# Performance work log

Measured on AMD Instinct MI355X. Metric: run time of the kernel, lower is better.

Reference implementation:

```python
import jax, jax.numpy as jnp
import numpy as np

B, S, D_IN, D_OUT = 4, 2048, 1024, 1024


def setup_inputs() -> dict:
    key = jax.random.key(0)
    k1, k2, k3, k4 = jax.random.split(key, 4)
    scale = 1.0 / np.sqrt(D_IN)
    return {
        "x": jax.random.normal(k1, (B, S, D_IN), dtype=jnp.float32),
        # torch nn.Linear weights have shape [d_out, d_in]
        "Wq": jax.random.normal(k2, (D_OUT, D_IN), dtype=jnp.float32) * scale,
        "Wk": jax.random.normal(k3, (D_OUT, D_IN), dtype=jnp.float32) * scale,
        "Wv": jax.random.normal(k4, (D_OUT, D_IN), dtype=jnp.float32) * scale,
    }


def reference(x, Wq, Wk, Wv):
    # Linear projections (torch Linear: y = x @ W.T), no bias
    q = jnp.einsum('bsd,od->bso', x, Wq)
    k = jnp.einsum('bsd,od->bso', x, Wk)
    v = jnp.einsum('bsd,od->bso', x, Wv)
    s = q.shape[1]
    scores = jnp.einsum('bqd,bkd->bqk', q, k)  # [B, S, S]
    causal = jnp.tril(jnp.ones((s, s), dtype=bool))  # True = keep
    scores = jnp.where(causal[None], scores, -jnp.inf)
    scale = jnp.asarray(k.shape[-1], scores.dtype) ** 0.5
    weights = jax.nn.softmax(scores / scale, axis=-1)
    return jnp.einsum('bqk,bkd->bqd', weights, v)
```

## Files before the change

kernel.cpp:

```cpp
#include <hip/hip_runtime.h>

#define BATCH 4
#define SEQ   2048
#define DIM   1024
#define MTOT  (BATCH * SEQ)
#define BK    32

typedef __bf16 bf16x8 __attribute__((ext_vector_type(8)));
typedef __bf16 bf16x4 __attribute__((ext_vector_type(4)));
typedef float  f32x4  __attribute__((ext_vector_type(4)));

#define VMCNT(N) asm volatile("s_waitcnt vmcnt(" #N ")" ::: "memory")

__device__ __forceinline__ void gl_lds16(const __bf16* g, __bf16* l) {
    __builtin_amdgcn_global_load_lds(
        (const __attribute__((address_space(1))) void*)g,
        (__attribute__((address_space(3))) void*)l,
        16, 0, 0);
}

__global__ __launch_bounds__(256) void cvt_all_kernel(
    const float* __restrict__ x,  const float* __restrict__ w0,
    const float* __restrict__ w1, const float* __restrict__ w2,
    __bf16* __restrict__ xd, __bf16* __restrict__ d0,
    __bf16* __restrict__ d1, __bf16* __restrict__ d2,
    float* __restrict__ sums)
{
    const int bid = blockIdx.x;
    if (bid >= 5632) {
        const int i = ((bid - 5632) * 256 + threadIdx.x) * 4;
        *(float4*)(sums + i) = (float4){0.f, 0.f, 0.f, 0.f};
        return;
    }
    const float* s;
    __bf16* d;
    int base;
    if (bid < 4096)      { s = x;  d = xd; base = bid; }
    else if (bid < 4608) { s = w0; d = d0; base = bid - 4096; }
    else if (bid < 5120) { s = w1; d = d1; base = bid - 4608; }
    else                 { s = w2; d = d2; base = bid - 5120; }
    const int i = (base * 256 + threadIdx.x) * 8;
    const float4 a = *(const float4*)(s + i);
    const float4 b = *(const float4*)(s + i + 4);
    bf16x8 o;
    o[0] = (__bf16)a.x; o[1] = (__bf16)a.y; o[2] = (__bf16)a.z; o[3] = (__bf16)a.w;
    o[4] = (__bf16)b.x; o[5] = (__bf16)b.y; o[6] = (__bf16)b.z; o[7] = (__bf16)b.w;
    *(bf16x8*)(d + i) = o;
}

__device__ __forceinline__ void gemm_core(
    const __bf16* __restrict__ A, size_t lda,
    const __bf16* __restrict__ Bm, size_t ldb,
    int m0, int n0, int kTiles,
    __bf16* lA, __bf16* lB,
    f32x4 (&acc)[4][4])
{
    const int tid  = threadIdx.x;
    const int lane = tid & 63;
    const int wave = tid >> 6;
    const int wm = (wave >> 1) << 6;
    const int wn = (wave & 1) << 6;

#pragma unroll
    for (int i = 0; i < 4; ++i)
#pragma unroll
        for (int j = 0; j < 4; ++j)
            acc[i][j] = (f32x4){0.f, 0.f, 0.f, 0.f};

    for (int kt = 0; kt < kTiles; ++kt) {
        const int k0 = kt << 5;
        __syncthreads();
#pragma unroll
        for (int it = 0; it < 2; ++it) {
            const int f   = tid + (it << 8);
            const int row = f >> 2;
            const int col = (f & 3) << 3;
            gl_lds16(A  + (size_t)(m0 + row) * lda + (size_t)(k0 + col), lA + f * 8);
            gl_lds16(Bm + (size_t)(n0 + row) * ldb + (size_t)(k0 + col), lB + f * 8);
        }
        __syncthreads();

        bf16x8 af[4], bfr[4];
#pragma unroll
        for (int i = 0; i < 4; ++i) {
            af[i]  = *(const bf16x8*)(lA + (size_t)(wm + i * 16 + (lane & 15)) * BK + ((lane >> 4) << 3));
            bfr[i] = *(const bf16x8*)(lB + (size_t)(wn + i * 16 + (lane & 15)) * BK + ((lane >> 4) << 3));
        }
#pragma unroll
        for (int i = 0; i < 4; ++i)
#pragma unroll
            for (int j = 0; j < 4; ++j)
                acc[i][j] = __builtin_amdgcn_mfma_f32_16x16x32_bf16(af[i], bfr[j], acc[i][j], 0, 0, 0);
    }
}

__device__ __forceinline__ void store_tile_bf16(
    f32x4 (&acc)[4][4], __bf16* scratch, bool transpose, float scale,
    __bf16* dst, size_t ldo, size_t r0, size_t c0,
    bool expMask = false, bool diag = false, float* sums = nullptr)
{
    const int tid  = threadIdx.x;
    const int lane = tid & 63;
    const int wave = tid >> 6;
    const int wm = (wave >> 1) << 6, wn = (wave & 1) << 6;
    const int quad = lane >> 4;
    const int ln15 = lane & 15;

#pragma unroll
    for (int p = 0; p < 4; ++p) {
        __syncthreads();
        if (!transpose) {
            if (wm == ((p >> 1) << 6)) {
#pragma unroll
                for (int ih = 0; ih < 2; ++ih) {
                    const int i = ((p & 1) << 1) + ih;
                    const int lr = ih * 16 + quad * 4;
#pragma unroll
                    for (int r = 0; r < 4; ++r) {
                        const int lm = wm + ((p & 1) << 5) + lr + r;
                        float ps = 0.f;
#pragma unroll
                        for (int j = 0; j < 4; ++j) {
                            const int ln = wn + j * 16 + ln15;
                            float v = acc[i][j][r] * scale;
                            if (expMask) {
                                v = (!diag || ln <= lm) ? __expf(v) : 0.f;
                            }
                            const __bf16 vb = (__bf16)v;
                            scratch[(lr + r) * 136 + ln] = vb;
                            ps += (float)vb;
                        }
                        if (sums) {
#pragma unroll
                            for (int off = 1; off < 16; off <<= 1)
                                ps += __shfl_xor(ps, off);
                            if (ln15 == 0)
                                atomicAdd(&sums[r0 + (p << 5) + lr + r], ps);
                        }
                    }
                }
            }
        } else {
            if (wn == ((p >> 1) << 6)) {
#pragma unroll
                for (int jh = 0; jh < 2; ++jh) {
                    const int j = ((p & 1) << 1) + jh;
                    const int lr = jh * 16 + ln15;
#pragma unroll
                    for (int i = 0; i < 4; ++i)
#pragma unroll
                        for (int r = 0; r < 4; ++r)
                            scratch[lr * 136 + wm + i * 16 + quad * 4 + r] =
                                (__bf16)(acc[i][j][r] * scale);
                }
            }
        }
        __syncthreads();
#pragma unroll
        for (int it = 0; it < 2; ++it) {
            const int g   = tid + (it << 8);
            const int row = g >> 4;
            const int col = (g & 15) << 3;
            *(bf16x8*)(dst + (r0 + p * 32 + row) * ldo + c0 + col) =
                *(const bf16x8*)(scratch + row * 136 + col);
        }
    }
}

__global__ __launch_bounds__(512, 2) void qkv_kernel(
    const __bf16* __restrict__ x,
    const __bf16* __restrict__ Wq,
    const __bf16* __restrict__ Wk,
    const __bf16* __restrict__ Wv,
    __bf16* __restrict__ Q, __bf16* __restrict__ Kb, __bf16* __restrict__ Vt)
{
    __shared__ __bf16 smem[49152];

    const int L  = blockIdx.x;
    const int g  = (L & 7) * 32 + (L >> 3);
    const int m0 = (g >> 3) << 8;
    const int B3 = g & 7;

    const int tid  = threadIdx.x;
    const int lane = tid & 63;
    const int ln15 = lane & 15;
    const int quad = lane >> 4;
    const int wave = tid >> 6;
    const int wm   = wave >> 1;
    const int wn   = wave & 1;

    const int r0  = tid >> 3;
    const int cst = ((((tid & 7) + 8) - (r0 & 7)) & 7) << 3;
    const int cq  = (((quad << 3) + ((ln15 & 7) << 3)) & 63);

    int aoff[4];
#pragma unroll
    for (int i = 0; i < 4; ++i)
        aoff[i] = ((wm >> 1) ? 8192 : 0) + (((wm & 1) << 6) + i * 16 + ln15) * 64 + cq;
    int boff[4];
#pragma unroll
    for (int j = 0; j < 4; ++j)
        boff[j] = 16384 + (wn ? 4096 : 0) + (j * 16 + ln15) * 64 + cq;

    const __bf16* Ab = x + (size_t)m0 * DIM;
    constexpr int nt = DIM / 64;

    for (int uu = 0; uu < 3; ++uu) {
        const int u  = B3 * 3 + uu;
        const int z  = u >> 3;
        const int n0 = (u & 7) << 7;
        const __bf16* W  = (z == 0) ? Wq : (z == 1) ? Wk : Wv;
        const __bf16* Bb = W + (size_t)n0 * DIM;

        f32x4 acc[4][4];
#pragma unroll
        for (int i = 0; i < 4; ++i)
#pragma unroll
            for (int j = 0; j < 4; ++j) acc[i][j] = (f32x4){0.f, 0.f, 0.f, 0.f};

#define SA(h, t) do {                                                         \
    const __bf16* gs_ = Ab + (size_t)((h) * 128 + r0) * DIM + ((t) << 6) + cst; \
    __bf16* ls_ = smem + (((t) & 1) * 24576 + (h) * 8192) + tid * 8;          \
    gl_lds16(gs_, ls_);                                                       \
    gl_lds16(gs_ + (size_t)64 * DIM, ls_ + 4096); } while (0)
#define SB(h, t) do {                                                         \
    const __bf16* gs_ = Bb + (size_t)((h) * 64 + r0) * DIM + ((t) << 6) + cst; \
    __bf16* ls_ = smem + (((t) & 1) * 24576 + 16384 + (h) * 4096) + tid * 8;  \
    gl_lds16(gs_, ls_); } while (0)

        bf16x8 aFa[4][2], aFb[4][2], bFr[2][2];
#define LDA_LO(DST, t) do { const __bf16* p_ = smem + ((t) & 1) * 24576;      \
    DST[0][0] = *(const bf16x8*)(p_ + aoff[0]);                               \
    DST[0][1] = *(const bf16x8*)(p_ + (aoff[0] ^ 32));                        \
    DST[1][0] = *(const bf16x8*)(p_ + aoff[1]);                               \
    DST[1][1] = *(const bf16x8*)(p_ + (aoff[1] ^ 32)); } while (0)
#define LDA_HI(DST, t) do { const __bf16* p_ = smem + ((t) & 1) * 24576;      \
    DST[2][0] = *(const bf16x8*)(p_ + aoff[2]);                               \
    DST[2][1] = *(const bf16x8*)(p_ + (aoff[2] ^ 32));                        \
    DST[3][0] = *(const bf16x8*)(p_ + aoff[3]);                               \
    DST[3][1] = *(const bf16x8*)(p_ + (aoff[3] ^ 32)); } while (0)
#define LDB(s, j, t) do { const __bf16* p_ = smem + ((t) & 1) * 24576;        \
    bFr[s][0] = *(const bf16x8*)(p_ + boff[j]);                               \
    bFr[s][1] = *(const bf16x8*)(p_ + (boff[j] ^ 32)); } while (0)
#define MG(j, s, AC) do {                                                     \
    __builtin_amdgcn_s_setprio(1);                                            \
    _Pragma("unroll") for (int i_ = 0; i_ < 4; ++i_) {                        \
        acc[i_][j] = __builtin_amdgcn_mfma_f32_16x16x32_bf16(                 \
            AC[i_][0], bFr[s][0], acc[i_][j], 0, 0, 0);                       \
        acc[i_][j] = __builtin_amdgcn_mfma_f32_16x16x32_bf16(                 \
            AC[i_][1], bFr[s][1], acc[i_][j], 0, 0, 0); }                     \
    __builtin_amdgcn_s_setprio(0); } while (0)

#define TILE(AC, AN, T) do {                                                  \
                       \
    LDB(1, 1, T);                                                             \
    if ((T) + 1 < nt) SB(0, (T) + 1);                                         \
    __builtin_amdgcn_s_barrier();                                             \
    MG(0, 0, AC);                                                             \
    __builtin_amdgcn_s_barrier();                                             \
      \
    LDB(0, 2, T);                                                             \
    if ((T) + 1 < nt) SB(1, (T) + 1);                                         \
    if ((T) + 2 < nt) SA(0, (T) + 2);                                         \
    if ((T) + 1 < nt) { if ((T) + 2 < nt) VMCNT(4); else VMCNT(2); }          \
    __builtin_amdgcn_s_barrier();                                             \
    MG(1, 1, AC);                                                             \
    __builtin_amdgcn_s_barrier();                                             \
      \
    LDB(1, 3, T);                                                             \
    if ((T) + 1 < nt) LDA_LO(AN, (T) + 1);                                    \
    if ((T) + 2 < nt) SA(1, (T) + 2);                                         \
    if ((T) + 1 < nt) { if ((T) + 2 < nt) VMCNT(5); else VMCNT(1); }          \
    __builtin_amdgcn_s_barrier();                                             \
    MG(2, 0, AC);                                                             \
    __builtin_amdgcn_s_barrier();                                             \
           \
    if ((T) + 1 < nt) { LDA_HI(AN, (T) + 1); LDB(0, 0, (T) + 1); }            \
    if ((T) + 1 < nt) { if ((T) + 2 < nt) VMCNT(4); else VMCNT(0); }          \
    __builtin_amdgcn_s_barrier();                                             \
    MG(3, 1, AC);                                                             \
    __builtin_amdgcn_s_barrier(); } while (0)

        SA(0, 0); SA(1, 0); SB(0, 0); SB(1, 0);
        SA(0, 1); SA(1, 1);
        VMCNT(4);
        __builtin_amdgcn_s_barrier();
        LDA_LO(aFa, 0); LDA_HI(aFa, 0); LDB(0, 0, 0);

#pragma unroll 1
        for (int T = 0; T < nt; T += 2) {
            TILE(aFa, aFb, T);
            TILE(aFb, aFa, T + 1);
        }
#undef SA
#undef SB
#undef LDA_LO
#undef LDA_HI
#undef LDB
#undef MG
#undef TILE

        __syncthreads();
        __bf16* scratch = smem;

        if (z < 2) {
            __bf16* dst = (z == 0) ? Q : Kb;
#pragma unroll
            for (int h = 0; h < 2; ++h) {
                if ((wm >> 1) == h) {
#pragma unroll
                    for (int i = 0; i < 4; ++i) {
                        const int lr = ((wm & 1) << 6) + i * 16 + quad * 4;
#pragma unroll
                        for (int j = 0; j < 4; ++j) {
                            const int lc = (wn << 6) + j * 16 + ln15;
#pragma unroll
                            for (int r = 0; r < 4; ++r)
                                scratch[(lr + r) * 136 + lc] = (__bf16)acc[i][j][r];
                        }
                    }
                }
                __syncthreads();
#pragma unroll
                for (int it = 0; it < 4; ++it) {
                    const int f = tid + (it << 9);
                    const int row = f >> 4, col = (f & 15) << 3;
                    *(bf16x8*)(dst + (size_t)(m0 + h * 128 + row) * DIM + n0 + col) =
                        *(const bf16x8*)(scratch + row * 136 + col);
                }
                __syncthreads();
            }
        } else {
            const size_t b  = (size_t)(m0 >> 11);
            const int  ms0  = m0 & (SEQ - 1);
            __bf16* dst = Vt + b * (size_t)DIM * SEQ;
#pragma unroll
            for (int i = 0; i < 4; ++i) {
                const int sl = (wm << 6) + i * 16 + quad * 4;
#pragma unroll
                for (int j = 0; j < 4; ++j) {
                    const int dl = (wn << 6) + j * 16 + ln15;
                    bf16x4 v;
#pragma unroll
                    for (int r = 0; r < 4; ++r) v[r] = (__bf16)acc[i][j][r];
                    *(bf16x4*)(scratch + dl * 264 + sl) = v;
                }
            }
            __syncthreads();
#pragma unroll
            for (int it = 0; it < 8; ++it) {
                const int f = tid + (it << 9);
                const int row = f >> 5, blk = f & 31;
                *(bf16x8*)(dst + (size_t)(n0 + row) * SEQ + ms0 + blk * 8) =
                    *(const bf16x8*)(scratch + row * 264 + blk * 8);
            }
            __syncthreads();
        }
    }
}

__global__ __launch_bounds__(256) void scores_kernel(
    const __bf16* __restrict__ Q, const __bf16* __restrict__ Kb,
    __bf16* __restrict__ Sc, float* __restrict__ sums)
{
    const int L = blockIdx.x;
    const int g = (L & 7) * 68 + (L >> 3);
    const int b = g / 136;
    const int t = g - b * 136;
    int i = (int)((sqrtf(8.f * t + 1.f) - 1.f) * 0.5f);
    while ((i + 1) * (i + 2) / 2 <= t) ++i;
    while (i * (i + 1) / 2 > t) --i;
    const int j = t - i * (i + 1) / 2;

    __shared__ __bf16 smem[8192];
    __bf16* lA = smem;
    __bf16* lB = smem + 128 * BK;
    const __bf16* A  = Q  + (size_t)b * SEQ * DIM;
    const __bf16* Bm = Kb + (size_t)b * SEQ * DIM;

    f32x4 acc[4][4];
    gemm_core(A, DIM, Bm, DIM, i << 7, j << 7, DIM / BK, lA, lB, acc);

    store_tile_bf16(acc, smem, false, 0.03125f,
                    Sc + (size_t)b * SEQ * SEQ, SEQ,
                    (size_t)(i << 7), (size_t)(j << 7),
                    true, (i == j),
                    sums + (size_t)b * SEQ);
}

__global__ __launch_bounds__(256) void pv_kernel(
    const __bf16* __restrict__ P, const __bf16* __restrict__ Vt,
    const float* __restrict__ sums, float* __restrict__ out)
{
    const int L = blockIdx.x;
    const int c = L & 7;
    const int k = L >> 3;
    const int b = c >> 1;
    const int i = 15 - (c & 1) - ((k >> 3) << 1);
    const int x = k & 7;

    __shared__ __bf16 smem[8192];
    __bf16* lA = smem;
    __bf16* lB = smem + 128 * BK;
    const __bf16* A  = P  + (size_t)b * SEQ * SEQ;
    const __bf16* Bm = Vt + (size_t)b * DIM * SEQ;

    f32x4 acc[4][4];
    gemm_core(A, SEQ, Bm, SEQ, i << 7, x << 7, (i + 1) * (128 / BK), lA, lB, acc);

    const int lane = threadIdx.x & 63;
    const int wave = threadIdx.x >> 6;
    const int wm = (wave >> 1) << 6, wn = (wave & 1) << 6;
#pragma unroll
    for (int ii = 0; ii < 4; ++ii)
#pragma unroll
        for (int jj = 0; jj < 4; ++jj)
#pragma unroll
            for (int r = 0; r < 4; ++r) {
                const int m = (i << 7) + wm + ii * 16 + ((lane >> 4) << 2) + r;
                const int n = (x << 7) + wn + jj * 16 + (lane & 15);
                out[((size_t)b * SEQ + m) * DIM + n] =
                    acc[ii][jj][r] / sums[(b << 11) + m];
            }
}

extern "C" void kernel_launch(void* const* d_in, const int* in_sizes, int n_in,
                              void* d_out, int out_size, void* d_ws, size_t ws_size,
                              hipStream_t stream) {
    const float* x  = (const float*)d_in[0];
    const float* Wq = (const float*)d_in[1];
    const float* Wk = (const float*)d_in[2];
    const float* Wv = (const float*)d_in[3];
    float* out = (float*)d_out;

    char* ws = (char*)d_ws;
    __bf16* Q  = (__bf16*)(ws);
    __bf16* Kb = (__bf16*)(ws + (16ull << 20));
    __bf16* Vt = (__bf16*)(ws + (32ull << 20));
    __bf16* Sc = (__bf16*)(ws + (48ull << 20));
    __bf16* Wqb = (__bf16*)(ws + (80ull << 20));
    __bf16* Wkb = (__bf16*)(ws + (82ull << 20));
    __bf16* Wvb = (__bf16*)(ws + (84ull << 20));
    float*  sums = (float*)(ws + (86ull << 20));
    __bf16* xb  = (__bf16*)d_out;

    cvt_all_kernel<<<dim3(5640), 256, 0, stream>>>(x, Wq, Wk, Wv, xb, Wqb, Wkb, Wvb, sums);

    qkv_kernel    <<<dim3(256),  512, 0, stream>>>(xb, Wqb, Wkb, Wvb, Q, Kb, Vt);
    scores_kernel <<<dim3(544),  256, 0, stream>>>(Q, Kb, Sc, sums);
    pv_kernel     <<<dim3(512),  256, 0, stream>>>(Sc, Vt, sums, out);
}
```

Before: 230.9 us.

## Move PV GEMM onto shared 256x128 pipelined unit_gemm with zeroed diagonal padding

Extracts the QKV kernel's 256x128 tile GEMM mainloop into a reusable unit_gemm with a simpler double-buffered schedule. The PV kernel now uses it, with 512-thread blocks and 256-row tiles that cover the causal range in 64-wide K steps. The convert kernel gains extra blocks that zero the upper-diagonal 128x128 score blocks, which the larger row tiles now read but scores_kernel never writes. The QKV mainloop loses its register double-buffered A fragments and finer interleaving, which may reduce its overlap.

```diff
diff --git a/kernel.cpp b/kernel.cpp
--- a/kernel.cpp
+++ b/kernel.cpp
@@ -24,9 +24,23 @@
     const float* __restrict__ w1, const float* __restrict__ w2,
     __bf16* __restrict__ xd, __bf16* __restrict__ d0,
     __bf16* __restrict__ d1, __bf16* __restrict__ d2,
-    float* __restrict__ sums)
+    float* __restrict__ sums, __bf16* __restrict__ Sc)
 {
     const int bid = blockIdx.x;
+    if (bid >= 5640) {
+        const int t  = bid - 5640;
+        const int bb = t >> 3, i2 = t & 7;
+        __bf16* base = Sc + (size_t)bb * SEQ * SEQ
+                          + (size_t)(i2 * 256) * SEQ + (i2 * 256 + 128);
+        const bf16x8 z8 = {};
+#pragma unroll
+        for (int it = 0; it < 8; ++it) {
+            const int row = it * 16 + (threadIdx.x >> 4);
+            const int col = (threadIdx.x & 15) << 3;
+            *(bf16x8*)(base + (size_t)row * SEQ + col) = z8;
+        }
+        return;
+    }
     if (bid >= 5632) {
         const int i = ((bid - 5632) * 256 + threadIdx.x) * 4;
         *(float4*)(sums + i) = (float4){0.f, 0.f, 0.f, 0.f};
@@ -167,20 +181,11 @@
     }
 }
 
-__global__ __launch_bounds__(512, 2) void qkv_kernel(
-    const __bf16* __restrict__ x,
-    const __bf16* __restrict__ Wq,
-    const __bf16* __restrict__ Wk,
-    const __bf16* __restrict__ Wv,
-    __bf16* __restrict__ Q, __bf16* __restrict__ Kb, __bf16* __restrict__ Vt)
-{
-    __shared__ __bf16 smem[49152];
-
-    const int L  = blockIdx.x;
-    const int g  = (L & 7) * 32 + (L >> 3);
-    const int m0 = (g >> 3) << 8;
-    const int B3 = g & 7;
-
+__device__ __forceinline__ void unit_gemm(
+    const __bf16* __restrict__ Ab, size_t lda,
+    const __bf16* __restrict__ Bb, size_t ldb,
+    int nt, __bf16* smem, f32x4 (&acc)[4][4])
+{
     const int tid  = threadIdx.x;
     const int lane = tid & 63;
     const int ln15 = lane & 15;
@@ -188,117 +193,115 @@
     const int wave = tid >> 6;
     const int wm   = wave >> 1;
     const int wn   = wave & 1;
-
-    const int r0  = tid >> 3;
-    const int cst = ((((tid & 7) + 8) - (r0 & 7)) & 7) << 3;
-    const int cq  = (((quad << 3) + ((ln15 & 7) << 3)) & 63);
-
-    int aoff[4];
+    const int r0   = tid >> 3;
+    const int cst  = ((((tid & 7) + 8) - (r0 & 7)) & 7) << 3;
+    const int cq   = (((quad << 3) + ((ln15 & 7) << 3)) & 63);
+
+    int aoff[4], boff[4];
+#pragma unroll
+    for (int i = 0; i < 4; ++i) aoff[i] = ((wm << 6) + i * 16 + ln15) * 64 + cq;
+#pragma unroll
+    for (int j = 0; j < 4; ++j) boff[j] = 16384 + ((wn << 6) + j * 16 + ln15) * 64 + cq;
+
 #pragma unroll
     for (int i = 0; i < 4; ++i)
-        aoff[i] = ((wm >> 1) ? 8192 : 0) + (((wm & 1) << 6) + i * 16 + ln15) * 64 + cq;
-    int boff[4];
-#pragma unroll
-    for (int j = 0; j < 4; ++j)
-        boff[j] = 16384 + (wn ? 4096 : 0) + (j * 16 + ln15) * 64 + cq;
+#pragma unroll
+        for (int j = 0; j < 4; ++j) acc[i][j] = (f32x4){0.f, 0.f, 0.f, 0.f};
+
+    bf16x8 aF[4][2], bFr[2][2];
+
+#define SA(h, t) do {                                                         \
+    const __bf16* gs_ = Ab + (size_t)((h) * 128 + r0) * lda + ((t) << 6) + cst; \
+    __bf16* ls_ = smem + (((t) & 1) * 24576 + (h) * 8192) + tid * 8;          \
+    gl_lds16(gs_, ls_);                                                       \
+    gl_lds16(gs_ + (size_t)64 * lda, ls_ + 4096); } while (0)
+#define SB(h, t) do {                                                         \
+    const __bf16* gs_ = Bb + (size_t)((h) * 64 + r0) * ldb + ((t) << 6) + cst; \
+    __bf16* ls_ = smem + (((t) & 1) * 24576 + 16384 + (h) * 4096) + tid * 8;  \
+    gl_lds16(gs_, ls_); } while (0)
+#define LDA_ALL(t) do { const __bf16* p_ = smem + ((t) & 1) * 24576;          \
+    _Pragma("unroll") for (int i_ = 0; i_ < 4; ++i_) {                        \
+        aF[i_][0] = *(const bf16x8*)(p_ + aoff[i_]);                          \
+        aF[i_][1] = *(const bf16x8*)(p_ + (aoff[i_] ^ 32)); } } while (0)
+#define LDB2(s, j, t) do { const __bf16* p_ = smem + ((t) & 1) * 24576;       \
+    bFr[s][0] = *(const bf16x8*)(p_ + boff[j]);                               \
+    bFr[s][1] = *(const bf16x8*)(p_ + (boff[j] ^ 32)); } while (0)
+#define MG(j, s) do {                                                         \
+    _Pragma("unroll") for (int i_ = 0; i_ < 4; ++i_) {                        \
+        acc[i_][j] = __builtin_amdgcn_mfma_f32_16x16x32_bf16(                 \
+            aF[i_][0], bFr[s][0], acc[i_][j], 0, 0, 0);                       \
+        acc[i_][j] = __builtin_amdgcn_mfma_f32_16x16x32_bf16(                 \
+            aF[i_][1], bFr[s][1], acc[i_][j], 0, 0, 0); } } while (0)
+
+    SA(0, 0); SA(1, 0); SB(0, 0); SB(1, 0);
+    SA(0, 1); SA(1, 1);
+    VMCNT(4);
+    __builtin_amdgcn_s_barrier();
+
+    for (int T = 0; T < nt; ++T) {
+        LDA_ALL(T);
+        LDB2(0, 0, T); LDB2(1, 1, T);
+        if (T + 1 < nt) {
+            SB(0, T + 1); SB(1, T + 1);
+            VMCNT(2);
+        }
+        __builtin_amdgcn_s_barrier();
+        __builtin_amdgcn_s_setprio(1);
+        MG(0, 0); MG(1, 1);
+        __builtin_amdgcn_s_setprio(0);
+        __builtin_amdgcn_s_barrier();
+        LDB2(0, 2, T); LDB2(1, 3, T);
+        if (T + 2 < nt) {
+            SA(0, T + 2); SA(1, T + 2);
+            VMCNT(4);
+        } else if (T + 1 < nt) {
+            VMCNT(0);
+        }
+        __builtin_amdgcn_s_barrier();
+        __builtin_amdgcn_s_setprio(1);
+        MG(2, 0); MG(3, 1);
+        __builtin_amdgcn_s_setprio(0);
+        __builtin_amdgcn_s_barrier();
+    }
+#undef SA
+#undef SB
+#undef LDA_ALL
+#undef LDB2
+#undef MG
+}
+
+__global__ __launch_bounds__(512, 2) void qkv_kernel(
+    const __bf16* __restrict__ x,
+    const __bf16* __restrict__ Wq,
+    const __bf16* __restrict__ Wk,
+    const __bf16* __restrict__ Wv,
+    __bf16* __restrict__ Q, __bf16* __restrict__ Kb, __bf16* __restrict__ Vt)
+{
+    __shared__ __bf16 smem[49152];
+
+    const int L  = blockIdx.x;
+    const int g  = (L & 7) * 32 + (L >> 3);
+    const int m0 = (g >> 3) << 8;
+    const int B3 = g & 7;
+
+    const int tid  = threadIdx.x;
+    const int lane = tid & 63;
+    const int ln15 = lane & 15;
+    const int quad = lane >> 4;
+    const int wave = tid >> 6;
+    const int wm   = wave >> 1;
+    const int wn   = wave & 1;
 
     const __bf16* Ab = x + (size_t)m0 * DIM;
-    constexpr int nt = DIM / 64;
 
     for (int uu = 0; uu < 3; ++uu) {
         const int u  = B3 * 3 + uu;
         const int z  = u >> 3;
         const int n0 = (u & 7) << 7;
         const __bf16* W  = (z == 0) ? Wq : (z == 1) ? Wk : Wv;
-        const __bf16* Bb = W + (size_t)n0 * DIM;
 
         f32x4 acc[4][4];
-#pragma unroll
-        for (int i = 0; i < 4; ++i)
-#pragma unroll
-            for (int j = 0; j < 4; ++j) acc[i][j] = (f32x4){0.f, 0.f, 0.f, 0.f};
-
-#define SA(h, t) do {                                                         \
-    const __bf16* gs_ = Ab + (size_t)((h) * 128 + r0) * DIM + ((t) << 6) + cst; \
-    __bf16* ls_ = smem + (((t) & 1) * 24576 + (h) * 8192) + tid * 8;          \
-    gl_lds16(gs_, ls_);                                                       \
-    gl_lds16(gs_ + (size_t)64 * DIM, ls_ + 4096); } while (0)
-#define SB(h, t) do {                                                         \
-    const __bf16* gs_ = Bb + (size_t)((h) * 64 + r0) * DIM + ((t) << 6) + cst; \
-    __bf16* ls_ = smem + (((t) & 1) * 24576 + 16384 + (h) * 4096) + tid * 8;  \
-    gl_lds16(gs_, ls_); } while (0)
-
-        bf16x8 aFa[4][2], aFb[4][2], bFr[2][2];
-#define LDA_LO(DST, t) do { const __bf16* p_ = smem + ((t) & 1) * 24576;      \
-    DST[0][0] = *(const bf16x8*)(p_ + aoff[0]);                               \
-    DST[0][1] = *(const bf16x8*)(p_ + (aoff[0] ^ 32));                        \
-    DST[1][0] = *(const bf16x8*)(p_ + aoff[1]);                               \
-    DST[1][1] = *(const bf16x8*)(p_ + (aoff[1] ^ 32)); } while (0)
-#define LDA_HI(DST, t) do { const __bf16* p_ = smem + ((t) & 1) * 24576;      \
-    DST[2][0] = *(const bf16x8*)(p_ + aoff[2]);                               \
-    DST[2][1] = *(const bf16x8*)(p_ + (aoff[2] ^ 32));                        \
-    DST[3][0] = *(const bf16x8*)(p_ + aoff[3]);                               \
-    DST[3][1] = *(const bf16x8*)(p_ + (aoff[3] ^ 32)); } while (0)
-#define LDB(s, j, t) do { const __bf16* p_ = smem + ((t) & 1) * 24576;        \
-    bFr[s][0] = *(const bf16x8*)(p_ + boff[j]);                               \
-    bFr[s][1] = *(const bf16x8*)(p_ + (boff[j] ^ 32)); } while (0)
-#define MG(j, s, AC) do {                                                     \
-    __builtin_amdgcn_s_setprio(1);                                            \
-    _Pragma("unroll") for (int i_ = 0; i_ < 4; ++i_) {                        \
-        acc[i_][j] = __builtin_amdgcn_mfma_f32_16x16x32_bf16(                 \
-            AC[i_][0], bFr[s][0], acc[i_][j], 0, 0, 0);                       \
-        acc[i_][j] = __builtin_amdgcn_mfma_f32_16x16x32_bf16(                 \
-            AC[i_][1], bFr[s][1], acc[i_][j], 0, 0, 0); }                     \
-    __builtin_amdgcn_s_setprio(0); } while (0)
-
-#define TILE(AC, AN, T) do {                                                  \
-                       \
-    LDB(1, 1, T);                                                             \
-    if ((T) + 1 < nt) SB(0, (T) + 1);                                         \
-    __builtin_amdgcn_s_barrier();                                             \
-    MG(0, 0, AC);                                                             \
-    __builtin_amdgcn_s_barrier();                                             \
-      \
-    LDB(0, 2, T);                                                             \
-    if ((T) + 1 < nt) SB(1, (T) + 1);                                         \
-    if ((T) + 2 < nt) SA(0, (T) + 2);                                         \
-    if ((T) + 1 < nt) { if ((T) + 2 < nt) VMCNT(4); else VMCNT(2); }          \
-    __builtin_amdgcn_s_barrier();                                             \
-    MG(1, 1, AC);                                                             \
-    __builtin_amdgcn_s_barrier();                                             \
-      \
-    LDB(1, 3, T);                                                             \
-    if ((T) + 1 < nt) LDA_LO(AN, (T) + 1);                                    \
-    if ((T) + 2 < nt) SA(1, (T) + 2);                                         \
-    if ((T) + 1 < nt) { if ((T) + 2 < nt) VMCNT(5); else VMCNT(1); }          \
-    __builtin_amdgcn_s_barrier();                                             \
-    MG(2, 0, AC);                                                             \
-    __builtin_amdgcn_s_barrier();                                             \
-           \
-    if ((T) + 1 < nt) { LDA_HI(AN, (T) + 1); LDB(0, 0, (T) + 1); }            \
-    if ((T) + 1 < nt) { if ((T) + 2 < nt) VMCNT(4); else VMCNT(0); }          \
-    __builtin_amdgcn_s_barrier();                                             \
-    MG(3, 1, AC);                                                             \
-    __builtin_amdgcn_s_barrier(); } while (0)
-
-        SA(0, 0); SA(1, 0); SB(0, 0); SB(1, 0);
-        SA(0, 1); SA(1, 1);
-        VMCNT(4);
-        __builtin_amdgcn_s_barrier();
-        LDA_LO(aFa, 0); LDA_HI(aFa, 0); LDB(0, 0, 0);
-
-#pragma unroll 1
-        for (int T = 0; T < nt; T += 2) {
-            TILE(aFa, aFb, T);
-            TILE(aFb, aFa, T + 1);
-        }
-#undef SA
-#undef SB
-#undef LDA_LO
-#undef LDA_HI
-#undef LDB
-#undef MG
-#undef TILE
+        unit_gemm(Ab, DIM, W + (size_t)n0 * DIM, DIM, DIM / 64, smem, acc);
 
         __syncthreads();
         __bf16* scratch = smem;
@@ -388,40 +391,44 @@
                     sums + (size_t)b * SEQ);
 }
 
-__global__ __launch_bounds__(256) void pv_kernel(
+__global__ __launch_bounds__(512, 2) void pv_kernel(
     const __bf16* __restrict__ P, const __bf16* __restrict__ Vt,
     const float* __restrict__ sums, float* __restrict__ out)
 {
-    const int L = blockIdx.x;
-    const int c = L & 7;
-    const int k = L >> 3;
-    const int b = c >> 1;
-    const int i = 15 - (c & 1) - ((k >> 3) << 1);
-    const int x = k & 7;
-
-    __shared__ __bf16 smem[8192];
-    __bf16* lA = smem;
-    __bf16* lB = smem + 128 * BK;
-    const __bf16* A  = P  + (size_t)b * SEQ * SEQ;
-    const __bf16* Bm = Vt + (size_t)b * DIM * SEQ;
+    __shared__ __bf16 smem[49152];
+
+    const int L  = blockIdx.x;
+    const int c  = L & 7;
+    const int k  = L >> 3;
+    const int b  = c >> 1;
+    const int i2 = 7 - (c & 1) - ((k >> 3) << 1);
+    const int xx = k & 7;
+
+    const __bf16* Ab = P  + (size_t)b * SEQ * SEQ + (size_t)(i2 << 8) * SEQ;
+    const __bf16* Bb = Vt + (size_t)b * DIM * SEQ + (size_t)(xx << 7) * SEQ;
 
     f32x4 acc[4][4];
-    gemm_core(A, SEQ, Bm, SEQ, i << 7, x << 7, (i + 1) * (128 / BK), lA, lB, acc);
-
-    const int lane = threadIdx.x & 63;
-    const int wave = threadIdx.x >> 6;
-    const int wm = (wave >> 1) << 6, wn = (wave & 1) << 6;
-#pragma unroll
-    for (int ii = 0; ii < 4; ++ii)
-#pragma unroll
-        for (int jj = 0; jj < 4; ++jj)
-#pragma unroll
-            for (int r = 0; r < 4; ++r) {
-                const int m = (i << 7) + wm + ii * 16 + ((lane >> 4) << 2) + r;
-                const int n = (x << 7) + wn + jj * 16 + (lane & 15);
-                out[((size_t)b * SEQ + m) * DIM + n] =
-                    acc[ii][jj][r] / sums[(b << 11) + m];
-            }
+    unit_gemm(Ab, SEQ, Bb, SEQ, (i2 + 1) << 2, smem, acc);
+
+    const int tid  = threadIdx.x;
+    const int lane = tid & 63;
+    const int ln15 = lane & 15;
+    const int quad = lane >> 4;
+    const int wave = tid >> 6;
+    const int wm   = wave >> 1;
+    const int wn   = wave & 1;
+
+#pragma unroll
+    for (int i = 0; i < 4; ++i)
+#pragma unroll
+        for (int r = 0; r < 4; ++r) {
+            const int m = (i2 << 8) + (wm << 6) + i * 16 + quad * 4 + r;
+            const float s = sums[(b << 11) + m];
+            float* orow = out + ((size_t)b * SEQ + m) * DIM + (xx << 7);
+#pragma unroll
+            for (int j = 0; j < 4; ++j)
+                orow[(wn << 6) + j * 16 + ln15] = acc[i][j][r] / s;
+        }
 }
 
 extern "C" void kernel_launch(void* const* d_in, const int* in_sizes, int n_in,
@@ -444,9 +451,10 @@
     float*  sums = (float*)(ws + (86ull << 20));
     __bf16* xb  = (__bf16*)d_out;
 
-    cvt_all_kernel<<<dim3(5640), 256, 0, stream>>>(x, Wq, Wk, Wv, xb, Wqb, Wkb, Wvb, sums);
+    cvt_all_kernel<<<dim3(5672), 256, 0, stream>>>(x, Wq, Wk, Wv, xb, Wqb, Wkb, Wvb,
+                                                   sums, Sc);
 
     qkv_kernel    <<<dim3(256),  512, 0, stream>>>(xb, Wqb, Wkb, Wvb, Q, Kb, Vt);
     scores_kernel <<<dim3(544),  256, 0, stream>>>(Q, Kb, Sc, sums);
-    pv_kernel     <<<dim3(512),  256, 0, stream>>>(Sc, Vt, sums, out);
-}
+    pv_kernel     <<<dim3(256),  512, 0, stream>>>(Sc, Vt, sums, out);
+}
```

Result: faster. 221.4 us (-4.1%).
